# Optimization experiments

Hardware: AMD Instinct MI355X
Metric: run time of the kernel (lower is better)

The kernel has to match this reference:

```python
import jax, jax.numpy as jnp
import numpy as np
import math

T, P, L, C, H, NPTS = 243, 17, 4, 128, 8, 4
DH = C // H


def _ln(x, g, b):
    m = jnp.mean(x, axis=-1, keepdims=True)
    v = jnp.mean((x - m) ** 2, axis=-1, keepdims=True)
    return (x - m) * jax.lax.rsqrt(v + 1e-5) * g + b


def _bilinear(v, grid):
    # v: [B, D, Hh, Ww]; grid: [B, Q, Pt, 2] in [-1,1], (x->W, y->H),
    # align_corners=False, zero padding (matches F.grid_sample in MSDeformAttn core)
    B, D, Hh, Ww = v.shape
    x = (grid[..., 0] + 1.0) * (Ww * 0.5) - 0.5
    y = (grid[..., 1] + 1.0) * (Hh * 0.5) - 0.5
    x0 = jnp.floor(x)
    y0 = jnp.floor(y)
    x0i = x0.astype(jnp.int32)
    y0i = y0.astype(jnp.int32)
    x1i = x0i + 1
    y1i = y0i + 1
    wx1 = x - x0
    wx0 = 1.0 - wx1
    wy1 = y - y0
    wy0 = 1.0 - wy1
    vf = v.reshape(B, D, Hh * Ww)
    Q, Pt = x.shape[1], x.shape[2]

    def gather(yi, xi):
        valid = ((yi >= 0) & (yi < Hh) & (xi >= 0) & (xi < Ww)).astype(v.dtype)
        idx = jnp.clip(yi, 0, Hh - 1) * Ww + jnp.clip(xi, 0, Ww - 1)
        g = jnp.take_along_axis(vf, idx.reshape(B, 1, Q * Pt), axis=2).reshape(B, D, Q, Pt)
        return g * valid[:, None]

    return (gather(y0i, x0i) * (wy0 * wx0)[:, None]
            + gather(y0i, x1i) * (wy0 * wx1)[:, None]
            + gather(y1i, x0i) * (wy1 * wx0)[:, None]
            + gather(y1i, x1i) * (wy1 * wx1)[:, None])  # [B, D, Q, Pt]


def _forward(x, ref_points, pe_buf, learn_pos, w_off, b_off, w_attn, b_attn,
             w_val, b_val, w_out, b_out, in_w, in_b, out_w, out_b,
             fc1_w, fc1_b, fc2_w, fc2_b, g1, be1, g2, be2, g3, be3):
    b, t, p, l, c = x.shape  # l = n_levels + 1
    Lq = t * p * L
    x0 = x[..., :1, :]
    xs = x[..., 1:, :].reshape(b, Lq, c)
    # --- subforward_self: norm_1 -> PE(query) -> MSDeformAttn ---
    xn = _ln(xs, g1, be1)
    q = (xn.reshape(b, t, p, L, c) + pe_buf + learn_pos).reshape(b, Lq, c)
    off = (q @ w_off.T + b_off).reshape(b, Lq, H, L, NPTS, 2)
    aw = jax.nn.softmax((q @ w_attn.T + b_attn).reshape(b, Lq, H, L * NPTS), axis=-1)
    aw = aw.reshape(b, Lq, H, L, NPTS)
    ref = jnp.broadcast_to(ref_points[:, :, :, None, :], (b, t, p, L, 2)).reshape(b, Lq, 2)
    normalizer = jnp.array([p, t], dtype=x.dtype)  # (W, H) per level
    loc = ref[:, :, None, None, None, :] + off / normalizer  # [b,Lq,H,L,Pt,2]
    grids = 2.0 * loc - 1.0
    val = (xn @ w_val.T + b_val).reshape(b, t, p, L, H, DH)
    v_maps = val.transpose(3, 0, 4, 5, 1, 2).reshape(L, b * H, DH, t, p)
    g = grids.transpose(3, 0, 2, 1, 4, 5).reshape(L, b * H, Lq, NPTS, 2)
    sampled = jax.vmap(_bilinear)(v_maps, g)  # [L, b*H, DH, Lq, Pt]
    aw_t = aw.transpose(3, 0, 2, 1, 4).reshape(L, b * H, 1, Lq, NPTS)
    o = jnp.sum(sampled * aw_t, axis=(0, 4))  # [b*H, DH, Lq]
    o = o.reshape(b, H, DH, Lq).transpose(0, 3, 1, 2).reshape(b, Lq, c)
    xs = (o @ w_out.T + b_out) + xs
    # --- concat level-0 back, cross (self) MHA over (p*l) tokens per frame ---
    xcat = jnp.concatenate([x0, xs.reshape(b, t, p, L, c)], axis=3).reshape(b * t, p * l, c)
    xn2 = _ln(xcat, g2, be2)
    qkv = xn2 @ in_w.T + in_b
    qh, kh, vh = jnp.split(qkv, 3, axis=-1)
    S = p * l
    qh = qh.reshape(b * t, S, H, DH)
    kh = kh.reshape(b * t, S, H, DH)
    vh = vh.reshape(b * t, S, H, DH)
    att = jax.nn.softmax(jnp.einsum('bqhd,bkhd->bhqk', qh, kh) / math.sqrt(DH), axis=-1)
    ca = jnp.einsum('bhqk,bkhd->bqhd', att, vh).reshape(b * t, S, c) @ out_w.T + out_b
    xcat = ca + xcat
    xr = xcat.reshape(b, t, p, l, c)
    # --- MLP block ---
    h = _ln(xr, g3, be3)
    h = jax.nn.gelu(h @ fc1_w.T + fc1_b, approximate=False) @ fc2_w.T + fc2_b
    return h + xr


def setup_inputs() -> dict:
    key = jax.random.key(0)
    ks = jax.random.split(key, 20)
    B = 2
    s = 0.02
    x = jax.random.normal(ks[0], (B, T, P, L + 1, C), jnp.float32)
    ref_points = jax.random.uniform(ks[1], (B, T, P, 2), dtype=jnp.float32)
    # sinusoidal PE buffer
    pos = np.arange(T, dtype=np.float32)[:, None]
    div = np.exp(np.arange(0, C, 2, dtype=np.float32) * (-math.log(10000.0) / C))
    ang = pos * div  # [T, C//2]
    pe = np.zeros((1, T, P, L, C), np.float32)
    pe[..., 0::2] = np.sin(ang)[None, :, None, None, :]
    pe[..., 1::2] = np.cos(ang)[None, :, None, None, :]
    rn = lambda k, shp: s * jax.random.normal(k, shp, jnp.float32)
    return {
        'x': x, 'ref_points': ref_points,
        'pe_buf': jnp.asarray(pe),
        'learn_pos': rn(ks[2], (1, T, P, L, C)),
        'w_off': rn(ks[3], (H * L * NPTS * 2, C)), 'b_off': rn(ks[4], (H * L * NPTS * 2,)),
        'w_attn': rn(ks[5], (H * L * NPTS, C)), 'b_attn': rn(ks[6], (H * L * NPTS,)),
        'w_val': rn(ks[7], (C, C)), 'b_val': rn(ks[8], (C,)),
        'w_out': rn(ks[9], (C, C)), 'b_out': rn(ks[10], (C,)),
        'in_w': rn(ks[11], (3 * C, C)), 'in_b': rn(ks[12], (3 * C,)),
        'out_w': rn(ks[13], (C, C)), 'out_b': rn(ks[14], (C,)),
        'fc1_w': rn(ks[15], (4 * C, C)), 'fc1_b': rn(ks[16], (4 * C,)),
        'fc2_w': rn(ks[17], (C, 4 * C)), 'fc2_b': rn(ks[18], (C,)),
        'g1': jnp.ones((C,), jnp.float32), 'be1': jnp.zeros((C,), jnp.float32),
        'g2': jnp.ones((C,), jnp.float32), 'be2': jnp.zeros((C,), jnp.float32),
        'g3': jnp.ones((C,), jnp.float32), 'be3': jnp.zeros((C,), jnp.float32),
    }


def reference(x, ref_points, pe_buf, learn_pos, w_off, b_off, w_attn, b_attn,
              w_val, b_val, w_out, b_out, in_w, in_b, out_w, out_b,
              fc1_w, fc1_b, fc2_w, fc2_b, g1, be1, g2, be2, g3, be3):
    return _forward(x, ref_points, pe_buf, learn_pos, w_off, b_off, w_attn, b_attn,
                    w_val, b_val, w_out, b_out, in_w, in_b, out_w, out_b,
                    fc1_w, fc1_b, fc2_w, fc2_b, g1, be1, g2, be2, g3, be3)
```

## Files before the change

### kernel.cpp

```cpp
#include <hip/hip_runtime.h>
#include <math.h>

#define T_ 243
#define P_ 17
#define L_ 4
#define C_ 128
#define H_ 8
#define NPTS_ 4
#define DH_ 16
#define B_ 2
#define LQ (T_*P_*L_)
#define NT1 (B_*LQ)
#define LL (L_+1)
#define S_ (P_*LL)
#define NT2 (B_*T_*P_*LL)

typedef __attribute__((ext_vector_type(8))) short short8v;
typedef __attribute__((ext_vector_type(4))) short short4v;
typedef __attribute__((ext_vector_type(4))) float float4v;

__device__ __forceinline__ unsigned short f2bf(float f){
  union { float f; unsigned u; } un; un.f = f;
  unsigned r = un.u + 0x7FFF + ((un.u >> 16) & 1);
  return (unsigned short)(r >> 16);
}
__device__ __forceinline__ float bf2f(unsigned short u){
  union { unsigned u; float f; } un; un.u = ((unsigned)u) << 16; return un.f;
}
__device__ __forceinline__ void dma16(const unsigned short* g, unsigned short* l){
  __builtin_amdgcn_global_load_lds(
      (const __attribute__((address_space(1))) void*)g,
      (__attribute__((address_space(3))) void*)l, 16, 0, 0);
}

__global__ void k_wcvt(const float* __restrict__ w0, const float* __restrict__ w1,
                       const float* __restrict__ w2, const float* __restrict__ w3,
                       const float* __restrict__ w4, const float* __restrict__ w5,
                       const float* __restrict__ w6, const float* __restrict__ w7,
                       unsigned short* __restrict__ dst){
  int i = blockIdx.x*256 + threadIdx.x;
  if (i >= 278528) return;
  float v;
  if      (i < 32768)  v = w0[i];
  else if (i < 49152)  v = w1[i-32768];
  else if (i < 65536)  v = w2[i-49152];
  else if (i < 81920)  v = w3[i-65536];
  else if (i < 131072) v = w4[i-81920];
  else if (i < 147456) v = w5[i-131072];
  else if (i < 212992) v = w6[i-147456];
  else                 v = w7[i-212992];
  dst[i] = f2bf(v);
}

__global__ __launch_bounds__(256) void k_ln1_q(
    const float* __restrict__ x, const float* __restrict__ pe,
    const float* __restrict__ lpos, const float* __restrict__ g1,
    const float* __restrict__ be1, unsigned short* __restrict__ xn,
    unsigned short* __restrict__ q) {
  int w = threadIdx.x >> 6; int lane = threadIdx.x & 63;
  int i = blockIdx.x*4 + w;
  int c = lane*2;
  int b = i / LQ; int r = i % LQ;
  int t = r / (P_*L_); int rp = r % (P_*L_);
  int p = rp / L_; int lv = rp % L_;
  const float* xrow = x + (((size_t)(b*T_+t)*P_ + p)*LL + 1 + lv)*C_;
  float2 v = *(const float2*)(xrow + c);
  float s1 = v.x + v.y, s2 = v.x*v.x + v.y*v.y;
  #pragma unroll
  for (int d=1; d<64; d<<=1){ s1 += __shfl_xor(s1,d); s2 += __shfl_xor(s2,d); }
  float mean = s1*(1.0f/C_);
  float var  = s2*(1.0f/C_) - mean*mean;
  float inv = rsqrtf(var + 1e-5f);
  float2 gg = *(const float2*)(g1 + c);
  float2 bb = *(const float2*)(be1 + c);
  float xn0 = (v.x - mean)*inv*gg.x + bb.x;
  float xn1 = (v.y - mean)*inv*gg.y + bb.y;
  size_t oi = (size_t)i*C_ + c;
  *(unsigned*)(xn + oi) = (unsigned)f2bf(xn0) | ((unsigned)f2bf(xn1) << 16);
  size_t pidx = (((size_t)t*P_ + p)*L_ + lv)*C_ + c;
  float2 pv = *(const float2*)(pe + pidx);
  float2 lp = *(const float2*)(lpos + pidx);
  *(unsigned*)(q + oi) = (unsigned)f2bf(xn0 + pv.x + lp.x) | ((unsigned)f2bf(xn1 + pv.y + lp.y) << 16);
}

__global__ __launch_bounds__(256) void k_x0ln(
    const float* __restrict__ x, const float* __restrict__ g2,
    const float* __restrict__ be2, float* __restrict__ xcat,
    unsigned short* __restrict__ xn2){
  int w = threadIdx.x >> 6; int lane = threadIdx.x & 63;
  int i = blockIdx.x*4 + w;
  if (i >= B_*T_*P_) return;
  int c = lane*2;
  size_t xrow = (size_t)i*LL;
  const float* xr = x + xrow*C_;
  float2 v = *(const float2*)(xr + c);
  float s1 = v.x + v.y, s2 = v.x*v.x + v.y*v.y;
  #pragma unroll
  for (int d=1; d<64; d<<=1){ s1 += __shfl_xor(s1,d); s2 += __shfl_xor(s2,d); }
  float mean = s1*(1.0f/C_);
  float var  = s2*(1.0f/C_) - mean*mean;
  float inv = rsqrtf(var + 1e-5f);
  float2 gg = *(const float2*)(g2 + c);
  float2 bb = *(const float2*)(be2 + c);
  *(float2*)(xcat + xrow*C_ + c) = v;
  float o0 = (v.x - mean)*inv*gg.x + bb.x;
  float o1 = (v.y - mean)*inv*gg.y + bb.y;
  *(unsigned*)(xn2 + xrow*C_ + c) = (unsigned)f2bf(o0) | ((unsigned)f2bf(o1) << 16);
}

template<int K, int N, int EPI>
__global__ __launch_bounds__(256) void k_mm(
    const unsigned short* __restrict__ A, const unsigned short* __restrict__ Bw,
    const float* __restrict__ bias, const float* __restrict__ res,
    float* __restrict__ outF, unsigned short* __restrict__ outB,
    const float* __restrict__ xres, const float* __restrict__ lng,
    const float* __restrict__ lnbe, int M)
{
  constexpr int NST = K / 128;
  __shared__ unsigned short As[64*128];
  __shared__ unsigned short Bs[128*128];
  int tid = threadIdx.x;
  int lane = tid & 63;
  int w = tid >> 6;
  int lr = lane & 15, kg = lane >> 4;
  int m0 = blockIdx.x * 64;
  int n0 = blockIdx.y * 128;
  int lrow = lane >> 4;
  int lch  = lane & 15;
  float4v acc[8] = {};
  for (int st = 0; st < NST; ++st){
    int kk = st*128;
    if (st) __syncthreads();
    #pragma unroll
    for (int j = 0; j < 4; ++j){
      int rb = w*16 + j*4;
      int srcch = lch ^ ((rb + lrow) & 7);
      dma16(A + (size_t)(m0 + rb + lrow)*K + kk + srcch*8, As + rb*128);
    }
    #pragma unroll
    for (int j = 0; j < 8; ++j){
      int rb = w*32 + j*4;
      int srcch = lch ^ ((rb + lrow) & 7);
      dma16(Bw + (size_t)(n0 + rb + lrow)*K + kk + srcch*8, Bs + rb*128);
    }
    __syncthreads();
    #pragma unroll
    for (int ks = 0; ks < 4; ++ks){
      int cn = ks*4 + kg;
      int arow = w*16 + lr;
      short8v af = *(const short8v*)(As + arow*128 + ((cn ^ (arow & 7)) * 8));
      #pragma unroll
      for (int nf = 0; nf < 8; ++nf){
        int brow = nf*16 + lr;
        short8v bf = *(const short8v*)(Bs + brow*128 + ((cn ^ (brow & 7)) * 8));
        acc[nf] = __builtin_amdgcn_mfma_f32_16x16x32_bf16(af, bf, acc[nf], 0, 0, 0);
      }
    }
  }
  #pragma unroll
  for (int j = 0; j < 4; ++j){
    int gr = m0 + w*16 + kg*4 + j;
    if (gr >= M) continue;
    if (EPI == 3 || EPI == 4 || EPI == 5){
      #pragma unroll
      for (int nf = 0; nf < 8; ++nf){
        int gc = n0 + nf*16 + lr;
        float v = acc[nf][j] + bias[gc];
        if (EPI == 3) {
          outF[(size_t)gr*N + gc] = v + res[(size_t)gr*N + gc];
        } else if (EPI == 4) {
          float gv = 0.5f*v*(1.0f + erff(v*0.70710678118654752440f));
          outB[(size_t)gr*N + gc] = f2bf(gv);
        } else {
          outB[(size_t)gr*N + gc] = f2bf(v);
        }
      }
    } else {
      size_t xrow;
      if (EPI == 6){
        int b = gr / LQ; int r = gr % LQ;
        int t = r / (P_*L_); int rp = r % (P_*L_);
        int p = rp / L_; int lv = rp % L_;
        xrow = (((size_t)(b*T_+t)*P_ + p)*LL) + 1 + lv;
      } else {
        xrow = (size_t)gr;
      }
      float vals[8];
      float s = 0.f, sq = 0.f;
      #pragma unroll
      for (int nf = 0; nf < 8; ++nf){
        int gc = n0 + nf*16 + lr;
        float v = acc[nf][j] + bias[gc];
        if (EPI == 6) v += xres[xrow*C_ + gc];
        else          v += res[xrow*C_ + gc];
        vals[nf] = v; s += v; sq += v*v;
      }
      #pragma unroll
      for (int d = 1; d < 16; d <<= 1){ s += __shfl_xor(s, d); sq += __shfl_xor(sq, d); }
      float mean = s*(1.0f/128.f);
      float varr = sq*(1.0f/128.f) - mean*mean;
      float linv = rsqrtf(varr + 1e-5f);
      #pragma unroll
      for (int nf = 0; nf < 8; ++nf){
        int gc = n0 + nf*16 + lr;
        outF[xrow*C_ + gc] = vals[nf];
        float ln = (vals[nf] - mean)*linv*lng[gc] + lnbe[gc];
        outB[xrow*C_ + gc] = f2bf(ln);
      }
    }
  }
}

__global__ __launch_bounds__(256) void k_mm3(
    const unsigned short* __restrict__ Aq, const unsigned short* __restrict__ Axn,
    const unsigned short* __restrict__ Bw,
    const float* __restrict__ b_off, const float* __restrict__ b_attn,
    const float* __restrict__ b_val,
    unsigned short* __restrict__ off_b, unsigned short* __restrict__ aw_b,
    unsigned short* __restrict__ vm_b, int M)
{
  __shared__ unsigned short As[64*128];
  __shared__ unsigned short Bs[128*128];
  int tid = threadIdx.x;
  int lane = tid & 63;
  int w = tid >> 6;
  int lr = lane & 15, kg = lane >> 4;
  int m0 = blockIdx.x * 64;
  int y  = blockIdx.y;
  int n0 = y * 128;
  const unsigned short* A = (y == 3) ? Axn : Aq;
  int lrow = lane >> 4;
  int lch  = lane & 15;
  float4v acc[8] = {};
  #pragma unroll
  for (int j = 0; j < 4; ++j){
    int rb = w*16 + j*4;
    int srcch = lch ^ ((rb + lrow) & 7);
    dma16(A + (size_t)(m0 + rb + lrow)*128 + srcch*8, As + rb*128);
  }
  #pragma unroll
  for (int j = 0; j < 8; ++j){
    int rb = w*32 + j*4;
    int srcch = lch ^ ((rb + lrow) & 7);
    dma16(Bw + (size_t)(n0 + rb + lrow)*128 + srcch*8, Bs + rb*128);
  }
  __syncthreads();
  #pragma unroll
  for (int ks = 0; ks < 4; ++ks){
    int cn = ks*4 + kg;
    int arow = w*16 + lr;
    short8v af = *(const short8v*)(As + arow*128 + ((cn ^ (arow & 7)) * 8));
    #pragma unroll
    for (int nf = 0; nf < 8; ++nf){
      int brow = nf*16 + lr;
      short8v bf = *(const short8v*)(Bs + brow*128 + ((cn ^ (brow & 7)) * 8));
      acc[nf] = __builtin_amdgcn_mfma_f32_16x16x32_bf16(af, bf, acc[nf], 0, 0, 0);
    }
  }
  const float* bias = (y < 2) ? b_off : (y == 2 ? b_attn - 256 : b_val - 384);
  #pragma unroll
  for (int j = 0; j < 4; ++j){
    int gr = m0 + w*16 + kg*4 + j;
    if (gr >= M) continue;
    #pragma unroll
    for (int nf = 0; nf < 8; ++nf){
      int gc = n0 + nf*16 + lr;
      float v = acc[nf][j] + bias[gc];
      unsigned short bv = f2bf(v);
      if (y < 2)      off_b[(size_t)gr*256 + gc]       = bv;
      else if (y==2)  aw_b [(size_t)gr*128 + gc - 256] = bv;
      else            vm_b [(size_t)gr*128 + gc - 384] = bv;
    }
  }
}

__global__ __launch_bounds__(256) void k_sample(
    const unsigned short* __restrict__ off, const unsigned short* __restrict__ awl,
    const float* __restrict__ refp, const unsigned short* __restrict__ vmap,
    unsigned short* __restrict__ o){
  int gid = blockIdx.x*256 + threadIdx.x;
  if (gid >= NT1*H_) return;
  int h = gid & 7; int i = gid >> 3;
  int b = i / LQ; int r = i % LQ;
  int t = r/(P_*L_); int rp = r%(P_*L_); int p = rp/L_;
  size_t rpi = (((size_t)b*T_+t)*P_+p)*2;
  float refx = refp[rpi + 0]*P_ - 0.5f;
  float refy = refp[rpi + 1]*T_ - 0.5f;

  float offv[32];
  {
    const short8v* op8 = (const short8v*)(off + (size_t)i*256 + h*32);
    #pragma unroll
    for (int s=0;s<4;++s){ short8v v = op8[s];
      #pragma unroll
      for (int j=0;j<8;++j) offv[s*8+j] = bf2f((unsigned short)v[j]); }
  }
  float awv[16];
  {
    const short8v* ap8 = (const short8v*)(awl + (size_t)i*128 + h*16);
    #pragma unroll
    for (int s=0;s<2;++s){ short8v v = ap8[s];
      #pragma unroll
      for (int j=0;j<8;++j) awv[s*8+j] = bf2f((unsigned short)v[j]); }
  }
  float m = awv[0];
  #pragma unroll
  for (int k=1;k<16;++k) m = fmaxf(m, awv[k]);
  float sum = 0.f;
  #pragma unroll
  for (int k=0;k<16;++k){ awv[k] = __expf(awv[k]-m); sum += awv[k]; }
  float inv = 1.f/sum;
  #pragma unroll
  for (int k=0;k<16;++k) awv[k] *= inv;

  float acc[16];
  #pragma unroll
  for (int d=0;d<16;++d) acc[d]=0.f;

  #pragma unroll
  for (int lv=0; lv<L_; ++lv){
    const unsigned short* vlv = vmap + ((size_t)b*LQ + lv)*128 + h*16;
    #pragma unroll
    for (int pt=0; pt<NPTS_; ++pt){
      float px = refx + offv[(lv*4+pt)*2+0];
      float py = refy + offv[(lv*4+pt)*2+1];
      float w  = awv[lv*4+pt];
      float fx = floorf(px), fy = floorf(py);
      int x0 = (int)fx, y0 = (int)fy;
      float wx1 = px - fx, wx0 = 1.f - wx1;
      float wy1 = py - fy, wy0 = 1.f - wy1;
      float cw[4] = {w*wy0*wx0, w*wy0*wx1, w*wy1*wx0, w*wy1*wx1};
      int ys[4] = {y0, y0, y0+1, y0+1};
      int xs[4] = {x0, x0+1, x0, x0+1};
      #pragma unroll
      for (int cidx=0; cidx<4; ++cidx){
        int yy = ys[cidx], xx = xs[cidx];
        if (yy>=0 && yy<T_ && xx>=0 && xx<P_){
          const short8v* vp = (const short8v*)(vlv + (size_t)(yy*P_ + xx)*(L_*128));
          short8v v0 = vp[0], v1 = vp[1];
          float wgt = cw[cidx];
          #pragma unroll
          for (int d=0;d<8;++d){
            acc[d]   = fmaf(wgt, bf2f((unsigned short)v0[d]), acc[d]);
            acc[8+d] = fmaf(wgt, bf2f((unsigned short)v1[d]), acc[8+d]);
          }
        }
      }
    }
  }
  short8v o0, o1;
  #pragma unroll
  for (int d=0;d<8;++d){ o0[d] = (short)f2bf(acc[d]); o1[d] = (short)f2bf(acc[8+d]); }
  short8v* op = (short8v*)(o + (size_t)i*C_ + h*DH_);
  op[0] = o0; op[1] = o1;
}

#define AT5_WAVE 5312
__global__ __launch_bounds__(128) void k_attn5(const unsigned short* __restrict__ qkv,
                                               unsigned short* __restrict__ ca){
  __shared__ unsigned short alds[2*AT5_WAVE];
  int w = threadIdx.x >> 6; int lane = threadIdx.x & 63;
  int bt = blockIdx.x >> 2; int hp = blockIdx.x & 3;
  int h = hp*2 + w;
  unsigned short* Kb = alds + w*AT5_WAVE;
  unsigned short* Vb = Kb + 1920;
  unsigned short* Pb = Kb + 3648;
  const unsigned short* base = qkv + (size_t)bt*85*384 + h*16;
  for (int idx = lane; idx < 192; idx += 64){
    int s = idx >> 1; int d0 = (idx & 1)*8;
    short8v kv = {}, vv = {};
    if (s < 85){
      const unsigned short* rp = base + (size_t)s*384 + d0;
      kv = *(const short8v*)(rp + 128);
      vv = *(const short8v*)(rp + 256);
    }
    *(short8v*)(Kb + s*20 + d0) = kv;
    #pragma unroll
    for (int j=0;j<8;++j) Vb[(d0+j)*108 + s] = (unsigned short)vv[j];
  }
  __syncthreads();
  int g = lane >> 4; int li = lane & 15;
  const short8v zero8 = {};
  short8v qf_cur = zero8;
  if (g < 2 && li < 85) qf_cur = *(const short8v*)(base + (size_t)li*384 + g*8);
  #pragma unroll 1
  for (int qt = 0; qt < 6; ++qt){
    short8v qf_next = zero8;
    int qn = (qt+1)*16 + li;
    if (qt < 5 && g < 2 && qn < 85)
      qf_next = *(const short8v*)(base + (size_t)qn*384 + g*8);
    float4v sc[6];
    #pragma unroll
    for (int kt = 0; kt < 6; ++kt){
      short8v kf = zero8;
      if (g < 2) kf = *(const short8v*)(Kb + (kt*16 + li)*20 + g*8);
      float4v z = {};
      sc[kt] = __builtin_amdgcn_mfma_f32_16x16x32_bf16(kf, qf_cur, z, 0, 0, 0);
    }
    float m = -1e30f;
    #pragma unroll
    for (int kt = 0; kt < 6; ++kt)
      #pragma unroll
      for (int j = 0; j < 4; ++j){
        float v = sc[kt][j]*0.25f;
        if (kt == 5 && (g*4 + j) >= 5) v = -1e30f;
        sc[kt][j] = v;
        m = fmaxf(m, v);
      }
    m = fmaxf(m, __shfl_xor(m, 16));
    m = fmaxf(m, __shfl_xor(m, 32));
    float sum = 0.f;
    #pragma unroll
    for (int kt = 0; kt < 6; ++kt){
      short4v pf;
      #pragma unroll
      for (int j = 0; j < 4; ++j){
        float e = __expf(sc[kt][j] - m);
        sum += e;
        pf[j] = (short)f2bf(e);
      }
      *(short4v*)(Pb + li*104 + kt*16 + g*4) = pf;
    }
    sum += __shfl_xor(sum, 16);
    sum += __shfl_xor(sum, 32);
    float inv = 1.f/sum;
    float4v oacc = {};
    #pragma unroll
    for (int kt32 = 0; kt32 < 3; ++kt32){
      short8v vf  = *(const short8v*)(Vb + li*108 + kt32*32 + g*8);
      short8v pf8 = *(const short8v*)(Pb + li*104 + kt32*32 + g*8);
      oacc = __builtin_amdgcn_mfma_f32_16x16x32_bf16(vf, pf8, oacc, 0, 0, 0);
    }
    int q = qt*16 + li;
    if (q < 85){
      short4v ov;
      #pragma unroll
      for (int j=0;j<4;++j) ov[j] = (short)f2bf(oacc[j]*inv);
      *(short4v*)(ca + ((size_t)bt*85 + q)*128 + h*16 + g*4) = ov;
    }
    qf_cur = qf_next;
  }
}

extern "C" void kernel_launch(void* const* d_in, const int* in_sizes, int n_in,
                              void* d_out, int out_size, void* d_ws, size_t ws_size,
                              hipStream_t stream) {
  (void)in_sizes; (void)n_in; (void)out_size; (void)ws_size;
  const float* x      = (const float*)d_in[0];
  const float* refp   = (const float*)d_in[1];
  const float* pe     = (const float*)d_in[2];
  const float* lpos   = (const float*)d_in[3];
  const float* w_off  = (const float*)d_in[4];
  const float* b_off  = (const float*)d_in[5];
  const float* w_attn = (const float*)d_in[6];
  const float* b_attn = (const float*)d_in[7];
  const float* w_val  = (const float*)d_in[8];
  const float* b_val  = (const float*)d_in[9];
  const float* w_out  = (const float*)d_in[10];
  const float* b_out  = (const float*)d_in[11];
  const float* in_w   = (const float*)d_in[12];
  const float* in_b   = (const float*)d_in[13];
  const float* out_w  = (const float*)d_in[14];
  const float* out_b  = (const float*)d_in[15];
  const float* fc1_w  = (const float*)d_in[16];
  const float* fc1_b  = (const float*)d_in[17];
  const float* fc2_w  = (const float*)d_in[18];
  const float* fc2_b  = (const float*)d_in[19];
  const float* g1     = (const float*)d_in[20];
  const float* be1    = (const float*)d_in[21];
  const float* g2     = (const float*)d_in[22];
  const float* be2    = (const float*)d_in[23];
  const float* g3     = (const float*)d_in[24];
  const float* be3    = (const float*)d_in[25];
  float* out = (float*)d_out;
  char* wsb = (char*)d_ws;

  unsigned short* xn_b  = (unsigned short*)(wsb + 0);
  unsigned short* q_b   = (unsigned short*)(wsb + 8460288);
  unsigned short* off_b = (unsigned short*)(wsb + 16920576);
  unsigned short* aw_b  = (unsigned short*)(wsb + 33841152);
  unsigned short* vm_b  = (unsigned short*)(wsb + 42301440);
  unsigned short* o_b   = (unsigned short*)(wsb + 50761728);
  float*          xcatB = (float*)(wsb + 59222016);
  unsigned short* xn2_b = (unsigned short*)(wsb + 80372736);
  unsigned short* qkv_b = (unsigned short*)(wsb + 90948096);
  unsigned short* wb    = (unsigned short*)(wsb + 122674176);
  unsigned short* ca_b  = (unsigned short*)(wsb + 0);
  unsigned short* ln3_b = (unsigned short*)(wsb + 80372736);
  unsigned short* hid_b = (unsigned short*)(wsb + 16920576);

  unsigned short* wb_off  = wb + 0;
  unsigned short* wb_wout = wb + 65536;
  unsigned short* wb_in   = wb + 81920;
  unsigned short* wb_outw = wb + 131072;
  unsigned short* wb_fc1  = wb + 147456;
  unsigned short* wb_fc2  = wb + 212992;

  const int GM1 = (NT1 + 63)/64;
  const int GM2 = (NT2 + 63)/64;

  hipLaunchKernelGGL(k_wcvt, dim3((278528+255)/256), dim3(256), 0, stream,
                     w_off, w_attn, w_val, w_out, in_w, out_w, fc1_w, fc2_w, wb);
  hipLaunchKernelGGL(k_ln1_q, dim3(NT1/4), dim3(256), 0, stream, x, pe, lpos, g1, be1, xn_b, q_b);
  hipLaunchKernelGGL(k_mm3, dim3(GM1,4), dim3(256), 0, stream,
                     q_b, xn_b, wb_off, b_off, b_attn, b_val, off_b, aw_b, vm_b, NT1);
  hipLaunchKernelGGL(k_sample, dim3((NT1*H_+255)/256), dim3(256), 0, stream,
                     off_b, aw_b, refp, vm_b, o_b);
  hipLaunchKernelGGL((k_mm<128,128,6>), dim3(GM1,1), dim3(256), 0, stream,
                     o_b, wb_wout, b_out, nullptr, xcatB, xn2_b, x, g2, be2, NT1);
  hipLaunchKernelGGL(k_x0ln, dim3((B_*T_*P_+3)/4), dim3(256), 0, stream, x, g2, be2, xcatB, xn2_b);
  hipLaunchKernelGGL((k_mm<128,384,5>), dim3(GM2,3), dim3(256), 0, stream,
                     xn2_b, wb_in, in_b, nullptr, nullptr, qkv_b, nullptr, nullptr, nullptr, NT2);
  hipLaunchKernelGGL(k_attn5, dim3(B_*T_*4), dim3(128), 0, stream, qkv_b, ca_b);
  hipLaunchKernelGGL((k_mm<128,128,7>), dim3(GM2,1), dim3(256), 0, stream,
                     ca_b, wb_outw, out_b, xcatB, xcatB, ln3_b, nullptr, g3, be3, NT2);
  hipLaunchKernelGGL((k_mm<128,512,4>), dim3(GM2,4), dim3(256), 0, stream,
                     ln3_b, wb_fc1, fc1_b, nullptr, nullptr, hid_b, nullptr, nullptr, nullptr, NT2);
  hipLaunchKernelGGL((k_mm<512,128,3>), dim3(GM2,1), dim3(256), 0, stream,
                     hid_b, wb_fc2, fc2_b, xcatB, out, nullptr, nullptr, nullptr, nullptr, NT2);
}
```

Before: 212.5 us.

## Fuse x0 layernorm into ln1 kernel and process two query tiles per attention iteration

The standalone x0 layernorm kernel is folded into the ln1/query kernel as extra rows, removing one launch. The attention kernel now handles two 16-query tiles per loop iteration with separate P buffers, interleaving independent MFMAs and softmax chains. It also raises wave priority around the MFMA sections. This adds LDS use and register pressure per wave, which may lower occupancy.

```diff
diff --git a/kernel.cpp b/kernel.cpp
--- a/kernel.cpp
+++ b/kernel.cpp
@@ -55,57 +55,54 @@
 __global__ __launch_bounds__(256) void k_ln1_q(
     const float* __restrict__ x, const float* __restrict__ pe,
     const float* __restrict__ lpos, const float* __restrict__ g1,
-    const float* __restrict__ be1, unsigned short* __restrict__ xn,
-    unsigned short* __restrict__ q) {
+    const float* __restrict__ be1, const float* __restrict__ g2,
+    const float* __restrict__ be2, unsigned short* __restrict__ xn,
+    unsigned short* __restrict__ q, float* __restrict__ xcat,
+    unsigned short* __restrict__ xn2) {
   int w = threadIdx.x >> 6; int lane = threadIdx.x & 63;
   int i = blockIdx.x*4 + w;
   int c = lane*2;
-  int b = i / LQ; int r = i % LQ;
-  int t = r / (P_*L_); int rp = r % (P_*L_);
-  int p = rp / L_; int lv = rp % L_;
-  const float* xrow = x + (((size_t)(b*T_+t)*P_ + p)*LL + 1 + lv)*C_;
-  float2 v = *(const float2*)(xrow + c);
-  float s1 = v.x + v.y, s2 = v.x*v.x + v.y*v.y;
-  #pragma unroll
-  for (int d=1; d<64; d<<=1){ s1 += __shfl_xor(s1,d); s2 += __shfl_xor(s2,d); }
-  float mean = s1*(1.0f/C_);
-  float var  = s2*(1.0f/C_) - mean*mean;
-  float inv = rsqrtf(var + 1e-5f);
-  float2 gg = *(const float2*)(g1 + c);
-  float2 bb = *(const float2*)(be1 + c);
-  float xn0 = (v.x - mean)*inv*gg.x + bb.x;
-  float xn1 = (v.y - mean)*inv*gg.y + bb.y;
-  size_t oi = (size_t)i*C_ + c;
-  *(unsigned*)(xn + oi) = (unsigned)f2bf(xn0) | ((unsigned)f2bf(xn1) << 16);
-  size_t pidx = (((size_t)t*P_ + p)*L_ + lv)*C_ + c;
-  float2 pv = *(const float2*)(pe + pidx);
-  float2 lp = *(const float2*)(lpos + pidx);
-  *(unsigned*)(q + oi) = (unsigned)f2bf(xn0 + pv.x + lp.x) | ((unsigned)f2bf(xn1 + pv.y + lp.y) << 16);
-}
-
-__global__ __launch_bounds__(256) void k_x0ln(
-    const float* __restrict__ x, const float* __restrict__ g2,
-    const float* __restrict__ be2, float* __restrict__ xcat,
-    unsigned short* __restrict__ xn2){
-  int w = threadIdx.x >> 6; int lane = threadIdx.x & 63;
-  int i = blockIdx.x*4 + w;
-  if (i >= B_*T_*P_) return;
-  int c = lane*2;
-  size_t xrow = (size_t)i*LL;
-  const float* xr = x + xrow*C_;
-  float2 v = *(const float2*)(xr + c);
-  float s1 = v.x + v.y, s2 = v.x*v.x + v.y*v.y;
-  #pragma unroll
-  for (int d=1; d<64; d<<=1){ s1 += __shfl_xor(s1,d); s2 += __shfl_xor(s2,d); }
-  float mean = s1*(1.0f/C_);
-  float var  = s2*(1.0f/C_) - mean*mean;
-  float inv = rsqrtf(var + 1e-5f);
-  float2 gg = *(const float2*)(g2 + c);
-  float2 bb = *(const float2*)(be2 + c);
-  *(float2*)(xcat + xrow*C_ + c) = v;
-  float o0 = (v.x - mean)*inv*gg.x + bb.x;
-  float o1 = (v.y - mean)*inv*gg.y + bb.y;
-  *(unsigned*)(xn2 + xrow*C_ + c) = (unsigned)f2bf(o0) | ((unsigned)f2bf(o1) << 16);
+  if (i < NT1){
+    int b = i / LQ; int r = i % LQ;
+    int t = r / (P_*L_); int rp = r % (P_*L_);
+    int p = rp / L_; int lv = rp % L_;
+    const float* xrow = x + (((size_t)(b*T_+t)*P_ + p)*LL + 1 + lv)*C_;
+    float2 v = *(const float2*)(xrow + c);
+    float s1 = v.x + v.y, s2 = v.x*v.x + v.y*v.y;
+    #pragma unroll
+    for (int d=1; d<64; d<<=1){ s1 += __shfl_xor(s1,d); s2 += __shfl_xor(s2,d); }
+    float mean = s1*(1.0f/C_);
+    float var  = s2*(1.0f/C_) - mean*mean;
+    float inv = rsqrtf(var + 1e-5f);
+    float2 gg = *(const float2*)(g1 + c);
+    float2 bb = *(const float2*)(be1 + c);
+    float xn0 = (v.x - mean)*inv*gg.x + bb.x;
+    float xn1 = (v.y - mean)*inv*gg.y + bb.y;
+    size_t oi = (size_t)i*C_ + c;
+    *(unsigned*)(xn + oi) = (unsigned)f2bf(xn0) | ((unsigned)f2bf(xn1) << 16);
+    size_t pidx = (((size_t)t*P_ + p)*L_ + lv)*C_ + c;
+    float2 pv = *(const float2*)(pe + pidx);
+    float2 lp = *(const float2*)(lpos + pidx);
+    *(unsigned*)(q + oi) = (unsigned)f2bf(xn0 + pv.x + lp.x) | ((unsigned)f2bf(xn1 + pv.y + lp.y) << 16);
+  } else {
+    int i0 = i - NT1;
+    if (i0 >= B_*T_*P_) return;
+    size_t xrow = (size_t)i0*LL;
+    const float* xr = x + xrow*C_;
+    float2 v = *(const float2*)(xr + c);
+    float s1 = v.x + v.y, s2 = v.x*v.x + v.y*v.y;
+    #pragma unroll
+    for (int d=1; d<64; d<<=1){ s1 += __shfl_xor(s1,d); s2 += __shfl_xor(s2,d); }
+    float mean = s1*(1.0f/C_);
+    float var  = s2*(1.0f/C_) - mean*mean;
+    float inv = rsqrtf(var + 1e-5f);
+    float2 gg = *(const float2*)(g2 + c);
+    float2 bb = *(const float2*)(be2 + c);
+    *(float2*)(xcat + xrow*C_ + c) = v;
+    float o0 = (v.x - mean)*inv*gg.x + bb.x;
+    float o1 = (v.y - mean)*inv*gg.y + bb.y;
+    *(unsigned*)(xn2 + xrow*C_ + c) = (unsigned)f2bf(o0) | ((unsigned)f2bf(o1) << 16);
+  }
 }
 
 template<int K, int N, int EPI>
@@ -355,16 +352,17 @@
   op[0] = o0; op[1] = o1;
 }
 
-#define AT5_WAVE 5312
-__global__ __launch_bounds__(128) void k_attn5(const unsigned short* __restrict__ qkv,
+#define AT6_WAVE 6976
+__global__ __launch_bounds__(128) void k_attn6(const unsigned short* __restrict__ qkv,
                                                unsigned short* __restrict__ ca){
-  __shared__ unsigned short alds[2*AT5_WAVE];
+  __shared__ unsigned short alds[2*AT6_WAVE];
   int w = threadIdx.x >> 6; int lane = threadIdx.x & 63;
   int bt = blockIdx.x >> 2; int hp = blockIdx.x & 3;
   int h = hp*2 + w;
-  unsigned short* Kb = alds + w*AT5_WAVE;
-  unsigned short* Vb = Kb + 1920;
-  unsigned short* Pb = Kb + 3648;
+  unsigned short* Kb  = alds + w*AT6_WAVE;
+  unsigned short* Vb  = Kb + 1920;
+  unsigned short* Pb0 = Kb + 3648;
+  unsigned short* Pb1 = Kb + 5312;
   const unsigned short* base = qkv + (size_t)bt*85*384 + h*16;
   for (int idx = lane; idx < 192; idx += 64){
     int s = idx >> 1; int d0 = (idx & 1)*8;
@@ -381,64 +379,84 @@
   __syncthreads();
   int g = lane >> 4; int li = lane & 15;
   const short8v zero8 = {};
-  short8v qf_cur = zero8;
-  if (g < 2 && li < 85) qf_cur = *(const short8v*)(base + (size_t)li*384 + g*8);
+  short8v qf0 = zero8, qf1 = zero8;
+  if (g < 2){
+    if (li < 85) qf0 = *(const short8v*)(base + (size_t)li*384 + g*8);
+    int q1i = 16 + li;
+    if (q1i < 85) qf1 = *(const short8v*)(base + (size_t)q1i*384 + g*8);
+  }
   #pragma unroll 1
-  for (int qt = 0; qt < 6; ++qt){
-    short8v qf_next = zero8;
-    int qn = (qt+1)*16 + li;
-    if (qt < 5 && g < 2 && qn < 85)
-      qf_next = *(const short8v*)(base + (size_t)qn*384 + g*8);
-    float4v sc[6];
+  for (int qp = 0; qp < 3; ++qp){
+    short8v qn0 = zero8, qn1 = zero8;
+    if (qp < 2 && g < 2){
+      int a = (qp+1)*32 + li, b2 = a + 16;
+      if (a  < 85) qn0 = *(const short8v*)(base + (size_t)a *384 + g*8);
+      if (b2 < 85) qn1 = *(const short8v*)(base + (size_t)b2*384 + g*8);
+    }
+    float4v sc0[6], sc1[6];
+    __builtin_amdgcn_s_setprio(1);
     #pragma unroll
     for (int kt = 0; kt < 6; ++kt){
       short8v kf = zero8;
       if (g < 2) kf = *(const short8v*)(Kb + (kt*16 + li)*20 + g*8);
       float4v z = {};
-      sc[kt] = __builtin_amdgcn_mfma_f32_16x16x32_bf16(kf, qf_cur, z, 0, 0, 0);
-    }
-    float m = -1e30f;
+      sc0[kt] = __builtin_amdgcn_mfma_f32_16x16x32_bf16(kf, qf0, z, 0, 0, 0);
+      sc1[kt] = __builtin_amdgcn_mfma_f32_16x16x32_bf16(kf, qf1, z, 0, 0, 0);
+    }
+    __builtin_amdgcn_s_setprio(0);
+    float m0 = -1e30f, m1 = -1e30f;
     #pragma unroll
     for (int kt = 0; kt < 6; ++kt)
       #pragma unroll
       for (int j = 0; j < 4; ++j){
-        float v = sc[kt][j]*0.25f;
-        if (kt == 5 && (g*4 + j) >= 5) v = -1e30f;
-        sc[kt][j] = v;
-        m = fmaxf(m, v);
-      }
-    m = fmaxf(m, __shfl_xor(m, 16));
-    m = fmaxf(m, __shfl_xor(m, 32));
-    float sum = 0.f;
+        bool msk = (kt == 5 && (g*4 + j) >= 5);
+        float v0 = sc0[kt][j]*0.25f; if (msk) v0 = -1e30f;
+        float v1 = sc1[kt][j]*0.25f; if (msk) v1 = -1e30f;
+        sc0[kt][j] = v0; m0 = fmaxf(m0, v0);
+        sc1[kt][j] = v1; m1 = fmaxf(m1, v1);
+      }
+    m0 = fmaxf(m0, __shfl_xor(m0, 16)); m1 = fmaxf(m1, __shfl_xor(m1, 16));
+    m0 = fmaxf(m0, __shfl_xor(m0, 32)); m1 = fmaxf(m1, __shfl_xor(m1, 32));
+    float sum0 = 0.f, sum1 = 0.f;
     #pragma unroll
     for (int kt = 0; kt < 6; ++kt){
-      short4v pf;
+      short4v p0, p1;
       #pragma unroll
       for (int j = 0; j < 4; ++j){
-        float e = __expf(sc[kt][j] - m);
-        sum += e;
-        pf[j] = (short)f2bf(e);
-      }
-      *(short4v*)(Pb + li*104 + kt*16 + g*4) = pf;
-    }
-    sum += __shfl_xor(sum, 16);
-    sum += __shfl_xor(sum, 32);
-    float inv = 1.f/sum;
-    float4v oacc = {};
+        float e0 = __expf(sc0[kt][j] - m0); sum0 += e0; p0[j] = (short)f2bf(e0);
+        float e1 = __expf(sc1[kt][j] - m1); sum1 += e1; p1[j] = (short)f2bf(e1);
+      }
+      *(short4v*)(Pb0 + li*104 + kt*16 + g*4) = p0;
+      *(short4v*)(Pb1 + li*104 + kt*16 + g*4) = p1;
+    }
+    sum0 += __shfl_xor(sum0, 16); sum1 += __shfl_xor(sum1, 16);
+    sum0 += __shfl_xor(sum0, 32); sum1 += __shfl_xor(sum1, 32);
+    float inv0 = 1.f/sum0, inv1 = 1.f/sum1;
+    float4v o0 = {}, o1 = {};
+    __builtin_amdgcn_s_setprio(1);
     #pragma unroll
     for (int kt32 = 0; kt32 < 3; ++kt32){
-      short8v vf  = *(const short8v*)(Vb + li*108 + kt32*32 + g*8);
-      short8v pf8 = *(const short8v*)(Pb + li*104 + kt32*32 + g*8);
-      oacc = __builtin_amdgcn_mfma_f32_16x16x32_bf16(vf, pf8, oacc, 0, 0, 0);
-    }
-    int q = qt*16 + li;
-    if (q < 85){
+      short8v vf  = *(const short8v*)(Vb  + li*108 + kt32*32 + g*8);
+      short8v p80 = *(const short8v*)(Pb0 + li*104 + kt32*32 + g*8);
+      short8v p81 = *(const short8v*)(Pb1 + li*104 + kt32*32 + g*8);
+      o0 = __builtin_amdgcn_mfma_f32_16x16x32_bf16(vf, p80, o0, 0, 0, 0);
+      o1 = __builtin_amdgcn_mfma_f32_16x16x32_bf16(vf, p81, o1, 0, 0, 0);
+    }
+    __builtin_amdgcn_s_setprio(0);
+    int q0 = qp*32 + li, q1 = q0 + 16;
+    if (q0 < 85){
       short4v ov;
       #pragma unroll
-      for (int j=0;j<4;++j) ov[j] = (short)f2bf(oacc[j]*inv);
-      *(short4v*)(ca + ((size_t)bt*85 + q)*128 + h*16 + g*4) = ov;
-    }
-    qf_cur = qf_next;
+      for (int j=0;j<4;++j) ov[j] = (short)f2bf(o0[j]*inv0);
+      *(short4v*)(ca + ((size_t)bt*85 + q0)*128 + h*16 + g*4) = ov;
+    }
+    if (q1 < 85){
+      short4v ov;
+      #pragma unroll
+      for (int j=0;j<4;++j) ov[j] = (short)f2bf(o1[j]*inv1);
+      *(short4v*)(ca + ((size_t)bt*85 + q1)*128 + h*16 + g*4) = ov;
+    }
+    qf0 = qn0; qf1 = qn1;
   }
 }
 
@@ -501,17 +519,17 @@
 
   hipLaunchKernelGGL(k_wcvt, dim3((278528+255)/256), dim3(256), 0, stream,
                      w_off, w_attn, w_val, w_out, in_w, out_w, fc1_w, fc2_w, wb);
-  hipLaunchKernelGGL(k_ln1_q, dim3(NT1/4), dim3(256), 0, stream, x, pe, lpos, g1, be1, xn_b, q_b);
+  hipLaunchKernelGGL(k_ln1_q, dim3((NT1 + B_*T_*P_ + 3)/4), dim3(256), 0, stream,
+                     x, pe, lpos, g1, be1, g2, be2, xn_b, q_b, xcatB, xn2_b);
   hipLaunchKernelGGL(k_mm3, dim3(GM1,4), dim3(256), 0, stream,
                      q_b, xn_b, wb_off, b_off, b_attn, b_val, off_b, aw_b, vm_b, NT1);
   hipLaunchKernelGGL(k_sample, dim3((NT1*H_+255)/256), dim3(256), 0, stream,
                      off_b, aw_b, refp, vm_b, o_b);
   hipLaunchKernelGGL((k_mm<128,128,6>), dim3(GM1,1), dim3(256), 0, stream,
                      o_b, wb_wout, b_out, nullptr, xcatB, xn2_b, x, g2, be2, NT1);
-  hipLaunchKernelGGL(k_x0ln, dim3((B_*T_*P_+3)/4), dim3(256), 0, stream, x, g2, be2, xcatB, xn2_b);
   hipLaunchKernelGGL((k_mm<128,384,5>), dim3(GM2,3), dim3(256), 0, stream,
                      xn2_b, wb_in, in_b, nullptr, nullptr, qkv_b, nullptr, nullptr, nullptr, NT2);
-  hipLaunchKernelGGL(k_attn5, dim3(B_*T_*4), dim3(128), 0, stream, qkv_b, ca_b);
+  hipLaunchKernelGGL(k_attn6, dim3(B_*T_*4), dim3(128), 0, stream, qkv_b, ca_b);
   hipLaunchKernelGGL((k_mm<128,128,7>), dim3(GM2,1), dim3(256), 0, stream,
                      ca_b, wb_outw, out_b, xcatB, xcatB, ln3_b, nullptr, g3, be3, NT2);
   hipLaunchKernelGGL((k_mm<128,512,4>), dim3(GM2,4), dim3(256), 0, stream,
```

Measured after the change: 204.0 us. 1.04x faster.
